# Performance work log

Hardware: AMD Instinct MI355X
Metric: run time of the kernel (lower is better)

Reference implementation:

```python
import jax, jax.numpy as jnp
import numpy as np


def setup_inputs() -> dict:
    key = jax.random.key(0)
    k1, k2 = jax.random.split(key)
    B, N, D = 16, 2048, 256
    candidate_vector = jax.random.normal(k1, (B, N, D), dtype=jnp.float32)
    # lengths in [1, N] so every softmax row has at least one valid column
    length = jax.random.randint(k2, (B,), 1, N + 1, dtype=jnp.int64)
    return {"candidate_vector": candidate_vector, "length": length}


def reference(candidate_vector, length):
    # scores[b,i,j] = <x_bi, x_bj>   (B, N, N)
    scores = jnp.einsum('bid,bjd->bij', candidate_vector, candidate_vector)
    # torch mask: mask[b,i,j] = (j < length[b]) -> columns past length masked
    N = candidate_vector.shape[1]
    col_valid = jnp.arange(N)[None, None, :] < length[:, None, None]  # (B,1,N)->(B,N,N) broadcast
    scores = jnp.where(col_valid, scores, -jnp.inf)
    weights = jax.nn.softmax(scores, axis=2)
    return jnp.einsum('bij,bjd->bid', weights, candidate_vector)
```

## Files before the change

kernel.cpp:

```cpp
#include <hip/hip_runtime.h>
#include <hip/hip_fp16.h>
#include <math.h>

typedef _Float16 f16;
typedef __attribute__((ext_vector_type(8))) _Float16 f16x8;
typedef __attribute__((ext_vector_type(4))) _Float16 f16x4;
typedef __attribute__((ext_vector_type(4))) float f32x4;

#define NB 16
#define NN 2048
#define ND 256
#define KVB 32
#define QB 64
#define XSZ ((size_t)NB * NN * ND)

__device__ __forceinline__ void gll16(const void* g, void* l) {
    __builtin_amdgcn_global_load_lds(
        (const __attribute__((address_space(1))) unsigned int*)g,
        (__attribute__((address_space(3))) unsigned int*)l, 16, 0, 0);
}

__device__ __forceinline__ long long len_at(const int* lenp, int b, bool is64) {
    return is64 ? ((const long long*)lenp)[b] : (long long)lenp[b];
}

__device__ __forceinline__ float bperm_f(int src_lane, float v) {
    return __int_as_float(__builtin_amdgcn_ds_bpermute(src_lane * 4, __float_as_int(v)));
}

__global__ __launch_bounds__(256)
void prep(const float* __restrict__ X, f16* __restrict__ Xh, f16* __restrict__ Xt)
{
    const int b  = blockIdx.z;
    const int n0 = blockIdx.x * 64;
    const int d0 = blockIdx.y * 64;
    const int t  = threadIdx.x;
    __shared__ f16 T[64][72];

    const float* Xb  = X  + ((size_t)b*NN + n0)*ND + d0;
    f16*         Xhb = Xh + ((size_t)b*NN + n0)*ND + d0;
    #pragma unroll
    for (int it = 0; it < 4; ++it) {
        int r  = it*16 + (t >> 4);
        int c4 = t & 15;
        float4 v = *(const float4*)(Xb + (size_t)r*ND + c4*4);
        f16x4 h; h[0]=(f16)v.x; h[1]=(f16)v.y; h[2]=(f16)v.z; h[3]=(f16)v.w;
        *(f16x4*)&Xhb[(size_t)r*ND + c4*4] = h;
        *(f16x4*)&T[r][c4*4] = h;
    }
    __syncthreads();
    f16* Xtb = Xt + ((size_t)b*ND + d0)*NN + n0;
    #pragma unroll
    for (int it = 0; it < 2; ++it) {
        int id = it*256 + t;
        int dr = id >> 3;
        int ch = id & 7;
        f16x8 v;
        #pragma unroll
        for (int u = 0; u < 8; ++u) v[u] = T[ch*8+u][dr];
        *(f16x8*)&Xtb[(size_t)dr*NN + ch*8] = v;
    }
}

__global__ __launch_bounds__(256, 2)
void attn8(const f16* __restrict__ Xh, const f16* __restrict__ Xt,
           const int* __restrict__ lenp,
           f16* __restrict__ Op, float* __restrict__ Sl)
{
    const int tid  = threadIdx.x;
    const int lane = tid & 63;
    const int w = tid >> 6;
    const int g = lane >> 4;
    const int c = lane & 15;

    const bool is64 = (lenp[1] == 0);
    long long Lv[NB];
    #pragma unroll
    for (int i = 0; i < NB; ++i) Lv[i] = len_at(lenp, i, is64);
    const int x   = blockIdx.x & 7;
    const int kk2 = blockIdx.x >> 3;
    const int h   = kk2 & 1;
    const int k2  = kk2 >> 1;
    const int wanted = (k2 < 32) ? x : (15 - x);
    const int qt  = k2 & 31;
    int bsel = 0; long long Lb = 1;
    #pragma unroll
    for (int bb = 0; bb < NB; ++bb) {
        int rk = 0;
        #pragma unroll
        for (int b2 = 0; b2 < NB; ++b2)
            rk += (Lv[b2] > Lv[bb]) || (Lv[b2] == Lv[bb] && b2 < bb);
        if (rk == wanted) { bsel = bb; Lb = Lv[bb]; }
    }
    const int nt  = (int)((Lb + KVB - 1) / KVB);
    const int nth = (h == 0) ? ((nt + 1) >> 1) : (nt >> 1);
    if (nth == 0) return;

    __shared__ f16 Kl[8192];
    __shared__ f16 Vl[8192];
    __shared__ f16 Pl[4][16*40];

    const char* xhb = (const char*)(Xh + (size_t)bsel*NN*ND);
    const char* xtb = (const char*)(Xt + (size_t)bsel*ND*NN);

    f16x8 qf[8];
    {
        const char* qp = xhb + (size_t)(qt*QB + w*16 + c)*512 + g*16;
        #pragma unroll
        for (int kk = 0; kk < 8; ++kk) qf[kk] = *(const f16x8*)(qp + kk*64);
    }

    auto stage_k = [&](int kv0) {
        char* kb = (char*)&Kl[0];
        #pragma unroll
        for (int it = 0; it < 4; ++it) {
            int S  = it*256 + tid;
            int kk = S >> 7, j = (S >> 2) & 31, gg = S & 3;
            gll16(xhb + (size_t)(kv0 + j)*512 + kk*64 + gg*16, kb + S*16);
        }
    };
    auto stage_v = [&](int kv0) {
        char* vb = (char*)&Vl[0];
        #pragma unroll
        for (int it = 0; it < 4; ++it) {
            int T  = it*256 + tid;
            int dt = T >> 6, cc = (T >> 2) & 15, gg = T & 3;
            gll16(xtb + (size_t)(dt*16 + cc)*4096 + (size_t)(kv0 + gg*8)*2, vb + T*16);
        }
    };

    f32x4 o[16];
    #pragma unroll
    for (int dt = 0; dt < 16; ++dt) o[dt] = (f32x4){0.f,0.f,0.f,0.f};
    float m = -INFINITY;
    float l = 0.f;

    f16* pw = &Pl[w][0];

    stage_k(h*KVB);
    stage_v(h*KVB);

    for (int ti = 0; ti < nth; ++ti) {
        const int kv0 = (2*ti + h) * KVB;
        const bool more = (ti + 1 < nth);

        asm volatile("s_waitcnt vmcnt(4)" ::: "memory");
        __builtin_amdgcn_s_barrier();

        const char* kb = (const char*)&Kl[0];
        const char* vb = (const char*)&Vl[0];

        f32x4 s0 = (f32x4){0.f,0.f,0.f,0.f};
        f32x4 s1 = (f32x4){0.f,0.f,0.f,0.f};
        __builtin_amdgcn_s_setprio(1);
        #pragma unroll
        for (int kk = 0; kk < 8; ++kk) {
            f16x8 b0 = *(const f16x8*)(kb + kk*2048        + c*64 + g*16);
            f16x8 b1 = *(const f16x8*)(kb + kk*2048 + 1024 + c*64 + g*16);
            s0 = __builtin_amdgcn_mfma_f32_16x16x32_f16(b0, qf[kk], s0, 0, 0, 0);
            s1 = __builtin_amdgcn_mfma_f32_16x16x32_f16(b1, qf[kk], s1, 0, 0, 0);
        }
        __builtin_amdgcn_s_setprio(0);

        asm volatile("s_waitcnt vmcnt(0)" ::: "memory");
        __builtin_amdgcn_s_barrier();
        if (more) stage_k(kv0 + 2*KVB);

        const float NEG = -1e30f;
        if (kv0 + KVB > (int)Lb) {
            const int jb = kv0 + g*4;
            #pragma unroll
            for (int r = 0; r < 4; ++r) {
                if (jb + r >= Lb)      s0[r] = NEG;
                if (jb + 16 + r >= Lb) s1[r] = NEG;
            }
        }

        float tm = fmaxf(fmaxf(fmaxf(s0[0],s0[1]), fmaxf(s0[2],s0[3])),
                         fmaxf(fmaxf(s1[0],s1[1]), fmaxf(s1[2],s1[3])));
        tm = fmaxf(tm, __shfl_xor(tm, 16, 64));
        tm = fmaxf(tm, __shfl_xor(tm, 32, 64));
        if (__any(tm > m + 8.f)) {
            float mn = fmaxf(m, tm);
            float sc = __expf(m - mn);
            m = mn; l *= sc;
            float scr[4];
            #pragma unroll
            for (int r = 0; r < 4; ++r) scr[r] = bperm_f(g*4 + r, sc);
            #pragma unroll
            for (int dt = 0; dt < 16; ++dt) {
                o[dt][0]*=scr[0]; o[dt][1]*=scr[1]; o[dt][2]*=scr[2]; o[dt][3]*=scr[3];
            }
        }
        float p0[4], p1[4];
        #pragma unroll
        for (int r = 0; r < 4; ++r) {
            p0[r] = __expf(s0[r] - m);
            p1[r] = __expf(s1[r] - m);
        }
        float rs = ((p0[0]+p0[1]) + (p0[2]+p0[3])) + ((p1[0]+p1[1]) + (p1[2]+p1[3]));
        rs += __shfl_xor(rs, 16, 64);
        rs += __shfl_xor(rs, 32, 64);
        l += rs;

        f16x4 pa, pb;
        pa[0]=(f16)p0[0]; pa[1]=(f16)p0[1]; pa[2]=(f16)p0[2]; pa[3]=(f16)p0[3];
        pb[0]=(f16)p1[0]; pb[1]=(f16)p1[1]; pb[2]=(f16)p1[2]; pb[3]=(f16)p1[3];
        *(f16x4*)&pw[c*40 + 4*g]      = pa;
        *(f16x4*)&pw[c*40 + 16 + 4*g] = pb;
        f16x8 pf = *(const f16x8*)&pw[c*40 + 8*g];

        __builtin_amdgcn_s_setprio(1);
        #pragma unroll
        for (int dt = 0; dt < 16; ++dt) {
            f16x8 vf = *(const f16x8*)(vb + dt*1024 + c*64 + g*16);
            o[dt] = __builtin_amdgcn_mfma_f32_16x16x32_f16(pf, vf, o[dt], 0, 0, 0);
        }
        __builtin_amdgcn_s_setprio(0);

        asm volatile("" ::: "memory");
        __builtin_amdgcn_s_barrier();
        if (more) stage_v(kv0 + 2*KVB);
    }

    float linv = 1.f / l;
    float inv[4];
    #pragma unroll
    for (int r = 0; r < 4; ++r) inv[r] = bperm_f(g*4 + r, linv);
    f16* op = Op + (size_t)h*XSZ + ((size_t)bsel*NN + (size_t)(qt*QB + w*16 + g*4))*ND + c;
    #pragma unroll
    for (int r = 0; r < 4; ++r) {
        #pragma unroll
        for (int dt = 0; dt < 16; ++dt)
            op[(size_t)r*ND + dt*16] = (f16)(o[dt][r] * inv[r]);
    }
    if (g == 0) {
        Sl[((size_t)(h*NB + bsel))*NN + (size_t)(qt*QB + w*16 + c)] = m + __logf(l);
    }
}

__global__ __launch_bounds__(256)
void merge(const f16* __restrict__ Op, const float* __restrict__ Sl,
           const int* __restrict__ lenp, float* __restrict__ out)
{
    const int tid = threadIdx.x;
    const int rg  = blockIdx.x * 8 + (tid >> 5);
    const int b   = rg >> 11;
    const int q   = rg & 2047;
    const int d0  = (tid & 31) * 8;

    const bool is64 = (lenp[1] == 0);
    const long long Lb = len_at(lenp, b, is64);

    const f16* p1 = Op + ((size_t)b*NN + q)*ND + d0;
    f16x8 a1 = *(const f16x8*)p1;
    float r[8];
    if (Lb <= KVB) {
        #pragma unroll
        for (int i = 0; i < 8; ++i) r[i] = (float)a1[i];
    } else {
        f16x8 a2 = *(const f16x8*)(p1 + XSZ);
        float s1 = Sl[(size_t)b*NN + q];
        float s2 = Sl[(size_t)(NB + b)*NN + q];
        float sm = fmaxf(s1, s2);
        float w1 = __expf(s1 - sm), w2 = __expf(s2 - sm);
        float dn = 1.f / (w1 + w2);
        w1 *= dn; w2 *= dn;
        #pragma unroll
        for (int i = 0; i < 8; ++i) r[i] = (float)a1[i]*w1 + (float)a2[i]*w2;
    }
    float* ob = out + ((size_t)b*NN + q)*ND + d0;
    *(float4*)ob       = (float4){r[0], r[1], r[2], r[3]};
    *(float4*)(ob + 4) = (float4){r[4], r[5], r[6], r[7]};
}

__global__ __launch_bounds__(256, 2)
void attn4(const f16* __restrict__ Xh, const f16* __restrict__ Xt,
           const int* __restrict__ lenp, float* __restrict__ out)
{
    const int tid  = threadIdx.x;
    const int lane = tid & 63;
    const int w = tid >> 6;
    const int g = lane >> 4;
    const int c = lane & 15;

    const bool is64 = (lenp[1] == 0);
    long long Lv[NB];
    #pragma unroll
    for (int i = 0; i < NB; ++i) Lv[i] = len_at(lenp, i, is64);
    const int x = blockIdx.x & 7;
    const int k = blockIdx.x >> 3;
    const int wanted = (k < 32) ? x : (15 - x);
    const int qt = k & 31;
    int bsel = 0; long long Lb = 1;
    #pragma unroll
    for (int bb = 0; bb < NB; ++bb) {
        int rk = 0;
        #pragma unroll
        for (int b2 = 0; b2 < NB; ++b2)
            rk += (Lv[b2] > Lv[bb]) || (Lv[b2] == Lv[bb] && b2 < bb);
        if (rk == wanted) { bsel = bb; Lb = Lv[bb]; }
    }
    const int nt = (int)((Lb + KVB - 1) / KVB);

    __shared__ f16 Kl[2][8192];
    __shared__ f16 Vl[2][8192];
    __shared__ f16 Pl[4][16*36];

    const char* xhb = (const char*)(Xh + (size_t)bsel*NN*ND);
    const char* xtb = (const char*)(Xt + (size_t)bsel*ND*NN);

    f16x8 qf[8];
    {
        const char* qp = xhb + (size_t)(qt*QB + w*16 + c)*512 + g*16;
        #pragma unroll
        for (int kk = 0; kk < 8; ++kk) qf[kk] = *(const f16x8*)(qp + kk*64);
    }

    auto stage = [&](int buf, int kv0) {
        char* kb = (char*)&Kl[buf][0];
        char* vb = (char*)&Vl[buf][0];
        #pragma unroll
        for (int it = 0; it < 4; ++it) {
            int S  = it*256 + tid;
            int kk = S >> 7, j = (S >> 2) & 31, gg = S & 3;
            gll16(xhb + (size_t)(kv0 + j)*512 + kk*64 + gg*16, kb + S*16);
        }
        #pragma unroll
        for (int it = 0; it < 4; ++it) {
            int T  = it*256 + tid;
            int dt = T >> 6, cc = (T >> 2) & 15, gg = T & 3;
            gll16(xtb + (size_t)(dt*16 + cc)*4096 + (size_t)(kv0 + gg*8)*2, vb + T*16);
        }
    };

    f32x4 o[16];
    #pragma unroll
    for (int dt = 0; dt < 16; ++dt) o[dt] = (f32x4){0.f,0.f,0.f,0.f};
    float m[4] = {-INFINITY,-INFINITY,-INFINITY,-INFINITY};
    float l[4] = {0.f,0.f,0.f,0.f};

    f16* pw = &Pl[w][0];

    stage(0, 0);
    if (nt > 1) stage(1, KVB);

    for (int t = 0; t < nt; ++t) {
        const int kv0 = t * KVB;
        const int buf = t & 1;

        if (t + 1 < nt) { asm volatile("s_waitcnt vmcnt(8)" ::: "memory"); }
        else            { asm volatile("s_waitcnt vmcnt(0)" ::: "memory"); }
        __builtin_amdgcn_s_barrier();

        const char* kb = (const char*)&Kl[buf][0];
        const char* vb = (const char*)&Vl[buf][0];

        f32x4 s0 = (f32x4){0.f,0.f,0.f,0.f};
        f32x4 s1 = (f32x4){0.f,0.f,0.f,0.f};
        #pragma unroll
        for (int kk = 0; kk < 8; ++kk) {
            f16x8 b0 = *(const f16x8*)(kb + kk*2048        + c*64 + g*16);
            f16x8 b1 = *(const f16x8*)(kb + kk*2048 + 1024 + c*64 + g*16);
            s0 = __builtin_amdgcn_mfma_f32_16x16x32_f16(qf[kk], b0, s0, 0, 0, 0);
            s1 = __builtin_amdgcn_mfma_f32_16x16x32_f16(qf[kk], b1, s1, 0, 0, 0);
        }

        const float NEG = -1e30f;
        if (kv0 + c >= Lb)      { s0[0]=NEG; s0[1]=NEG; s0[2]=NEG; s0[3]=NEG; }
        if (kv0 + 16 + c >= Lb) { s1[0]=NEG; s1[1]=NEG; s1[2]=NEG; s1[3]=NEG; }

        float mx[4], mn[4], sc[4], p0[4], p1[4], rs[4];
        #pragma unroll
        for (int r = 0; r < 4; ++r) mx[r] = fmaxf(s0[r], s1[r]);
        #pragma unroll
        for (int off = 8; off >= 1; off >>= 1) {
            #pragma unroll
            for (int r = 0; r < 4; ++r)
                mx[r] = fmaxf(mx[r], __shfl_xor(mx[r], off, 64));
        }
        #pragma unroll
        for (int r = 0; r < 4; ++r) {
            mn[r] = fmaxf(m[r], mx[r]);
            sc[r] = __expf(m[r] - mn[r]);
            p0[r] = __expf(s0[r] - mn[r]);
            p1[r] = __expf(s1[r] - mn[r]);
            rs[r] = p0[r] + p1[r];
        }
        #pragma unroll
        for (int off = 8; off >= 1; off >>= 1) {
            #pragma unroll
            for (int r = 0; r < 4; ++r)
                rs[r] += __shfl_xor(rs[r], off, 64);
        }
        bool chg = (sc[0]!=1.f) | (sc[1]!=1.f) | (sc[2]!=1.f) | (sc[3]!=1.f);
        if (__any(chg)) {
            #pragma unroll
            for (int dt = 0; dt < 16; ++dt) {
                o[dt][0]*=sc[0]; o[dt][1]*=sc[1]; o[dt][2]*=sc[2]; o[dt][3]*=sc[3];
            }
        }
        #pragma unroll
        for (int r = 0; r < 4; ++r) { l[r] = l[r]*sc[r] + rs[r]; m[r] = mn[r]; }

        #pragma unroll
        for (int r = 0; r < 4; ++r) {
            pw[(g*4+r)*36 + c]      = (f16)p0[r];
            pw[(g*4+r)*36 + 16 + c] = (f16)p1[r];
        }
        union { f16x4 hh[2]; f16x8 v; } pu;
        pu.hh[0] = *(const f16x4*)(pw + c*36 + g*8);
        pu.hh[1] = *(const f16x4*)(pw + c*36 + g*8 + 4);
        f16x8 pf = pu.v;

        #pragma unroll
        for (int dt = 0; dt < 16; ++dt) {
            f16x8 vf = *(const f16x8*)(vb + dt*1024 + c*64 + g*16);
            o[dt] = __builtin_amdgcn_mfma_f32_16x16x32_f16(pf, vf, o[dt], 0, 0, 0);
        }

        __builtin_amdgcn_s_barrier();
        if (t + 2 < nt) stage(buf, kv0 + 2*KVB);
    }

    float inv[4];
    #pragma unroll
    for (int r = 0; r < 4; ++r) inv[r] = 1.0f / l[r];
    float* ob = out + ((size_t)bsel*NN + (size_t)(qt*QB + w*16 + g*4))*ND + c;
    #pragma unroll
    for (int r = 0; r < 4; ++r) {
        #pragma unroll
        for (int dt = 0; dt < 16; ++dt)
            ob[(size_t)r*ND + dt*16] = o[dt][r] * inv[r];
    }
}

__global__ __launch_bounds__(256, 2)
void attn_fb(const float* __restrict__ X,
             const int* __restrict__ lenp,
             float* __restrict__ out)
{
    const int b   = blockIdx.y;
    const int qt  = blockIdx.x;
    const int tid = threadIdx.x;
    const int lane = tid & 63;
    const int w = tid >> 6;
    const int g = lane >> 4;
    const int c = lane & 15;

    const bool is64 = (lenp[1] == 0);
    const long long Lb = len_at(lenp, b, is64);

    __shared__ f16 Kl[KVB][264];
    __shared__ f16 Vt2[ND][40];
    __shared__ f16 Pl[4][16][40];

    const float* Xb = X + (size_t)b * NN * ND;

    f16x8 qf[8];
    {
        const float* qp = Xb + (size_t)(qt*64 + w*16 + c) * ND + g*8;
        #pragma unroll
        for (int kk = 0; kk < 8; ++kk) {
            float4 a = *(const float4*)(qp + kk*32);
            float4 d = *(const float4*)(qp + kk*32 + 4);
            f16x8 v;
            v[0]=(f16)a.x; v[1]=(f16)a.y; v[2]=(f16)a.z; v[3]=(f16)a.w;
            v[4]=(f16)d.x; v[5]=(f16)d.y; v[6]=(f16)d.z; v[7]=(f16)d.w;
            qf[kk] = v;
        }
    }

    f32x4 o[16];
    #pragma unroll
    for (int dt = 0; dt < 16; ++dt) o[dt] = (f32x4){0.f,0.f,0.f,0.f};
    float m[4] = {-INFINITY,-INFINITY,-INFINITY,-INFINITY};
    float lr[4] = {0.f,0.f,0.f,0.f};

    const int ntiles = (int)((Lb + KVB - 1) / KVB);
    for (int t = 0; t < ntiles; ++t) {
        const int kv0 = t * KVB;
        __syncthreads();
        #pragma unroll
        for (int it = 0; it < 8; ++it) {
            int idx4 = it*256 + tid;
            int row  = idx4 >> 6;
            int c4   = idx4 & 63;
            float4 v = *(const float4*)(Xb + (size_t)(kv0 + row)*ND + c4*4);
            f16x4 hh; hh[0]=(f16)v.x; hh[1]=(f16)v.y; hh[2]=(f16)v.z; hh[3]=(f16)v.w;
            *(f16x4*)&Kl[row][c4*4] = hh;
        }
        {
            const float* cp = Xb + (size_t)kv0*ND + tid;
            #pragma unroll
            for (int kq = 0; kq < 8; ++kq) {
                f16x4 hh;
                #pragma unroll
                for (int u = 0; u < 4; ++u) hh[u] = (f16)cp[(size_t)(kq*4+u)*ND];
                *(f16x4*)&Vt2[tid][kq*4] = hh;
            }
        }
        __syncthreads();

        f32x4 s0 = (f32x4){0.f,0.f,0.f,0.f};
        f32x4 s1 = (f32x4){0.f,0.f,0.f,0.f};
        #pragma unroll
        for (int kk = 0; kk < 8; ++kk) {
            f16x8 b0 = *(const f16x8*)&Kl[c     ][kk*32 + g*8];
            f16x8 b1 = *(const f16x8*)&Kl[16 + c][kk*32 + g*8];
            s0 = __builtin_amdgcn_mfma_f32_16x16x32_f16(qf[kk], b0, s0, 0, 0, 0);
            s1 = __builtin_amdgcn_mfma_f32_16x16x32_f16(qf[kk], b1, s1, 0, 0, 0);
        }

        const float NEG = -1e30f;
        if (kv0 + c >= Lb)      { s0[0]=NEG; s0[1]=NEG; s0[2]=NEG; s0[3]=NEG; }
        if (kv0 + 16 + c >= Lb) { s1[0]=NEG; s1[1]=NEG; s1[2]=NEG; s1[3]=NEG; }

        float mx[4], mn[4], sc[4], p0[4], p1[4], rs[4];
        #pragma unroll
        for (int r = 0; r < 4; ++r) mx[r] = fmaxf(s0[r], s1[r]);
        #pragma unroll
        for (int off = 8; off >= 1; off >>= 1) {
            #pragma unroll
            for (int r = 0; r < 4; ++r)
                mx[r] = fmaxf(mx[r], __shfl_xor(mx[r], off, 64));
        }
        #pragma unroll
        for (int r = 0; r < 4; ++r) {
            mn[r] = fmaxf(m[r], mx[r]);
            sc[r] = __expf(m[r] - mn[r]);
            p0[r] = __expf(s0[r] - mn[r]);
            p1[r] = __expf(s1[r] - mn[r]);
            rs[r] = p0[r] + p1[r];
        }
        #pragma unroll
        for (int off = 8; off >= 1; off >>= 1) {
            #pragma unroll
            for (int r = 0; r < 4; ++r)
                rs[r] += __shfl_xor(rs[r], off, 64);
        }
        bool chg = (sc[0]!=1.f) | (sc[1]!=1.f) | (sc[2]!=1.f) | (sc[3]!=1.f);
        if (__any(chg)) {
            #pragma unroll
            for (int dt = 0; dt < 16; ++dt) {
                o[dt][0]*=sc[0]; o[dt][1]*=sc[1]; o[dt][2]*=sc[2]; o[dt][3]*=sc[3];
            }
        }
        #pragma unroll
        for (int r = 0; r < 4; ++r) { lr[r] = lr[r]*sc[r] + rs[r]; m[r] = mn[r]; }

        #pragma unroll
        for (int r = 0; r < 4; ++r) {
            Pl[w][g*4+r][c]      = (f16)p0[r];
            Pl[w][g*4+r][16 + c] = (f16)p1[r];
        }
        f16x8 pf = *(const f16x8*)&Pl[w][c][g*8];

        #pragma unroll
        for (int dt = 0; dt < 16; ++dt) {
            f16x8 vf = *(const f16x8*)&Vt2[dt*16 + c][g*8];
            o[dt] = __builtin_amdgcn_mfma_f32_16x16x32_f16(pf, vf, o[dt], 0, 0, 0);
        }
    }

    float inv[4];
    #pragma unroll
    for (int r = 0; r < 4; ++r) inv[r] = 1.0f / lr[r];
    float* ob = out + ((size_t)b*NN + (size_t)(qt*64 + w*16 + g*4))*ND + c;
    #pragma unroll
    for (int r = 0; r < 4; ++r) {
        #pragma unroll
        for (int dt = 0; dt < 16; ++dt)
            ob[(size_t)r*ND + dt*16] = o[dt][r] * inv[r];
    }
}

extern "C" void kernel_launch(void* const* d_in, const int* in_sizes, int n_in,
                              void* d_out, int out_size, void* d_ws, size_t ws_size,
                              hipStream_t stream) {
    const float* X    = (const float*)d_in[0];
    const int*   lenp = (const int*)d_in[1];
    float*       out  = (float*)d_out;

    const size_t need_base  = XSZ * 2 * 2;
    const size_t need_split = need_base + XSZ * 2 * 2
                              + (size_t)2 * NB * NN * 4;
    if (ws_size >= need_split) {
        f16* Xh = (f16*)d_ws;
        f16* Xt = Xh + XSZ;
        f16* Op = Xt + XSZ;
        float* Sl = (float*)(Op + 2*XSZ);
        hipLaunchKernelGGL(prep, dim3(NN/64, ND/64, NB), dim3(256), 0, stream, X, Xh, Xt);
        hipLaunchKernelGGL(attn8, dim3(1024), dim3(256), 0, stream, Xh, Xt, lenp, Op, Sl);
        hipLaunchKernelGGL(merge, dim3(NB*NN/8), dim3(256), 0, stream, Op, Sl, lenp, out);
    } else if (ws_size >= need_base) {
        f16* Xh = (f16*)d_ws;
        f16* Xt = Xh + XSZ;
        hipLaunchKernelGGL(prep, dim3(NN/64, ND/64, NB), dim3(256), 0, stream, X, Xh, Xt);
        hipLaunchKernelGGL(attn4, dim3(512), dim3(256), 0, stream, Xh, Xt, lenp, out);
    } else {
        hipLaunchKernelGGL(attn_fb, dim3(NN/64, NB), dim3(256), 0, stream, X, lenp, out);
    }
}
```

Measured before the change: 96.57 us.

## Switch split-KV attention to 32x32x16 MFMA tiles with register P exchange

Replaces the 16x16x32 MFMA attention kernel with one built on 32x32x16 MFMAs. Each wave now owns 32 query rows, so a block covers 128 queries and the grid is halved to 512 blocks with launch bounds of one block per SM. The K/V LDS staging layouts are changed to match, and the probability matrix is exchanged between half-waves with cross-lane shuffles instead of going through LDS. The goal is fewer LDS reads per FLOP and no P round-trip through LDS, at the cost of higher register pressure (more Q fragments and accumulators) and less parallelism and occupancy.

```diff
diff --git a/kernel.cpp b/kernel.cpp
--- a/kernel.cpp
+++ b/kernel.cpp
@@ -6,12 +6,13 @@
 typedef __attribute__((ext_vector_type(8))) _Float16 f16x8;
 typedef __attribute__((ext_vector_type(4))) _Float16 f16x4;
 typedef __attribute__((ext_vector_type(4))) float f32x4;
+typedef __attribute__((ext_vector_type(16))) float f32x16;
+typedef unsigned int u32;
 
 #define NB 16
 #define NN 2048
 #define ND 256
 #define KVB 32
-#define QB 64
 #define XSZ ((size_t)NB * NN * ND)
 
 __device__ __forceinline__ void gll16(const void* g, void* l) {
@@ -62,16 +63,16 @@
     }
 }
 
-__global__ __launch_bounds__(256, 2)
-void attn8(const f16* __restrict__ Xh, const f16* __restrict__ Xt,
+__global__ __launch_bounds__(256, 1)
+void attn9(const f16* __restrict__ Xh, const f16* __restrict__ Xt,
            const int* __restrict__ lenp,
            f16* __restrict__ Op, float* __restrict__ Sl)
 {
     const int tid  = threadIdx.x;
     const int lane = tid & 63;
-    const int w = tid >> 6;
-    const int g = lane >> 4;
-    const int c = lane & 15;
+    const int w  = tid >> 6;
+    const int cl = lane & 31;
+    const int hi = lane >> 5;
 
     const bool is64 = (lenp[1] == 0);
     long long Lv[NB];
@@ -81,8 +82,8 @@
     const int kk2 = blockIdx.x >> 3;
     const int h   = kk2 & 1;
     const int k2  = kk2 >> 1;
-    const int wanted = (k2 < 32) ? x : (15 - x);
-    const int qt  = k2 & 31;
+    const int wanted = (k2 < 16) ? x : (15 - x);
+    const int qt  = k2 & 15;
     int bsel = 0; long long Lb = 1;
     #pragma unroll
     for (int bb = 0; bb < NB; ++bb) {
@@ -98,16 +99,17 @@
 
     __shared__ f16 Kl[8192];
     __shared__ f16 Vl[8192];
-    __shared__ f16 Pl[4][16*40];
 
     const char* xhb = (const char*)(Xh + (size_t)bsel*NN*ND);
     const char* xtb = (const char*)(Xt + (size_t)bsel*ND*NN);
 
-    f16x8 qf[8];
+    const int q0 = qt*128 + w*32;
+
+    f16x8 qf[16];
     {
-        const char* qp = xhb + (size_t)(qt*QB + w*16 + c)*512 + g*16;
-        #pragma unroll
-        for (int kk = 0; kk < 8; ++kk) qf[kk] = *(const f16x8*)(qp + kk*64);
+        const char* qp = xhb + (size_t)(q0 + cl)*512 + hi*16;
+        #pragma unroll
+        for (int kk = 0; kk < 16; ++kk) qf[kk] = *(const f16x8*)(qp + kk*32);
     }
 
     auto stage_k = [&](int kv0) {
@@ -115,8 +117,8 @@
         #pragma unroll
         for (int it = 0; it < 4; ++it) {
             int S  = it*256 + tid;
-            int kk = S >> 7, j = (S >> 2) & 31, gg = S & 3;
-            gll16(xhb + (size_t)(kv0 + j)*512 + kk*64 + gg*16, kb + S*16);
+            int kk = S >> 6, j = (S >> 1) & 31, h2 = S & 1;
+            gll16(xhb + (size_t)(kv0 + j)*512 + kk*32 + h2*16, kb + S*16);
         }
     };
     auto stage_v = [&](int kv0) {
@@ -124,18 +126,20 @@
         #pragma unroll
         for (int it = 0; it < 4; ++it) {
             int T  = it*256 + tid;
-            int dt = T >> 6, cc = (T >> 2) & 15, gg = T & 3;
-            gll16(xtb + (size_t)(dt*16 + cc)*4096 + (size_t)(kv0 + gg*8)*2, vb + T*16);
+            int ds = T >> 6, cc = (T >> 1) & 31, h2 = T & 1;
+            int dt = ds >> 1, s = ds & 1;
+            gll16(xtb + (size_t)(dt*32 + cc)*4096 + (size_t)(kv0 + s*16 + h2*8)*2,
+                  vb + T*16);
         }
     };
 
-    f32x4 o[16];
-    #pragma unroll
-    for (int dt = 0; dt < 16; ++dt) o[dt] = (f32x4){0.f,0.f,0.f,0.f};
+    f32x16 o[8];
+    #pragma unroll
+    for (int dt = 0; dt < 8; ++dt)
+        #pragma unroll
+        for (int r = 0; r < 16; ++r) o[dt][r] = 0.f;
     float m = -INFINITY;
     float l = 0.f;
-
-    f16* pw = &Pl[w][0];
 
     stage_k(h*KVB);
     stage_v(h*KVB);
@@ -150,15 +154,14 @@
         const char* kb = (const char*)&Kl[0];
         const char* vb = (const char*)&Vl[0];
 
-        f32x4 s0 = (f32x4){0.f,0.f,0.f,0.f};
-        f32x4 s1 = (f32x4){0.f,0.f,0.f,0.f};
+        f32x16 st;
+        #pragma unroll
+        for (int r = 0; r < 16; ++r) st[r] = 0.f;
         __builtin_amdgcn_s_setprio(1);
         #pragma unroll
-        for (int kk = 0; kk < 8; ++kk) {
-            f16x8 b0 = *(const f16x8*)(kb + kk*2048        + c*64 + g*16);
-            f16x8 b1 = *(const f16x8*)(kb + kk*2048 + 1024 + c*64 + g*16);
-            s0 = __builtin_amdgcn_mfma_f32_16x16x32_f16(b0, qf[kk], s0, 0, 0, 0);
-            s1 = __builtin_amdgcn_mfma_f32_16x16x32_f16(b1, qf[kk], s1, 0, 0, 0);
+        for (int kk = 0; kk < 16; ++kk) {
+            f16x8 ka = *(const f16x8*)(kb + kk*1024 + cl*32 + hi*16);
+            st = __builtin_amdgcn_mfma_f32_32x32x16_f16(ka, qf[kk], st, 0, 0, 0);
         }
         __builtin_amdgcn_s_setprio(0);
 
@@ -168,53 +171,67 @@
 
         const float NEG = -1e30f;
         if (kv0 + KVB > (int)Lb) {
-            const int jb = kv0 + g*4;
-            #pragma unroll
-            for (int r = 0; r < 4; ++r) {
-                if (jb + r >= Lb)      s0[r] = NEG;
-                if (jb + 16 + r >= Lb) s1[r] = NEG;
+            #pragma unroll
+            for (int r = 0; r < 16; ++r) {
+                int j = kv0 + (r & 3) + 8*(r >> 2) + 4*hi;
+                if (j >= (int)Lb) st[r] = NEG;
             }
         }
 
-        float tm = fmaxf(fmaxf(fmaxf(s0[0],s0[1]), fmaxf(s0[2],s0[3])),
-                         fmaxf(fmaxf(s1[0],s1[1]), fmaxf(s1[2],s1[3])));
-        tm = fmaxf(tm, __shfl_xor(tm, 16, 64));
+        float tm = st[0];
+        #pragma unroll
+        for (int r = 1; r < 16; ++r) tm = fmaxf(tm, st[r]);
         tm = fmaxf(tm, __shfl_xor(tm, 32, 64));
         if (__any(tm > m + 8.f)) {
             float mn = fmaxf(m, tm);
             float sc = __expf(m - mn);
             m = mn; l *= sc;
-            float scr[4];
-            #pragma unroll
-            for (int r = 0; r < 4; ++r) scr[r] = bperm_f(g*4 + r, sc);
-            #pragma unroll
-            for (int dt = 0; dt < 16; ++dt) {
-                o[dt][0]*=scr[0]; o[dt][1]*=scr[1]; o[dt][2]*=scr[2]; o[dt][3]*=scr[3];
-            }
-        }
-        float p0[4], p1[4];
-        #pragma unroll
-        for (int r = 0; r < 4; ++r) {
-            p0[r] = __expf(s0[r] - m);
-            p1[r] = __expf(s1[r] - m);
-        }
-        float rs = ((p0[0]+p0[1]) + (p0[2]+p0[3])) + ((p1[0]+p1[1]) + (p1[2]+p1[3]));
-        rs += __shfl_xor(rs, 16, 64);
+            float scr[16];
+            #pragma unroll
+            for (int r = 0; r < 16; ++r)
+                scr[r] = bperm_f((r & 3) + 8*(r >> 2) + 4*hi, sc);
+            #pragma unroll
+            for (int dt = 0; dt < 8; ++dt)
+                #pragma unroll
+                for (int r = 0; r < 16; ++r) o[dt][r] *= scr[r];
+        }
+        float p[16];
+        float rs = 0.f;
+        #pragma unroll
+        for (int r = 0; r < 16; ++r) { p[r] = __expf(st[r] - m); rs += p[r]; }
         rs += __shfl_xor(rs, 32, 64);
         l += rs;
 
-        f16x4 pa, pb;
-        pa[0]=(f16)p0[0]; pa[1]=(f16)p0[1]; pa[2]=(f16)p0[2]; pa[3]=(f16)p0[3];
-        pb[0]=(f16)p1[0]; pb[1]=(f16)p1[1]; pb[2]=(f16)p1[2]; pb[3]=(f16)p1[3];
-        *(f16x4*)&pw[c*40 + 4*g]      = pa;
-        *(f16x4*)&pw[c*40 + 16 + 4*g] = pb;
-        f16x8 pf = *(const f16x8*)&pw[c*40 + 8*g];
+        u32 pk[8];
+        #pragma unroll
+        for (int Q = 0; Q < 4; ++Q) {
+            f16x4 t;
+            t[0]=(f16)p[4*Q+0]; t[1]=(f16)p[4*Q+1];
+            t[2]=(f16)p[4*Q+2]; t[3]=(f16)p[4*Q+3];
+            pk[2*Q]   = ((u32*)&t)[0];
+            pk[2*Q+1] = ((u32*)&t)[1];
+        }
+        u32 rx0 = __shfl_xor(hi ? pk[0] : pk[2], 32, 64);
+        u32 rx1 = __shfl_xor(hi ? pk[1] : pk[3], 32, 64);
+        u32 rx2 = __shfl_xor(hi ? pk[4] : pk[6], 32, 64);
+        u32 rx3 = __shfl_xor(hi ? pk[5] : pk[7], 32, 64);
+        union { u32 u[4]; f16x8 v; } pf0, pf1;
+        pf0.u[0] = hi ? rx0 : pk[0];
+        pf0.u[1] = hi ? rx1 : pk[1];
+        pf0.u[2] = hi ? pk[2] : rx0;
+        pf0.u[3] = hi ? pk[3] : rx1;
+        pf1.u[0] = hi ? rx2 : pk[4];
+        pf1.u[1] = hi ? rx3 : pk[5];
+        pf1.u[2] = hi ? pk[6] : rx2;
+        pf1.u[3] = hi ? pk[7] : rx3;
 
         __builtin_amdgcn_s_setprio(1);
         #pragma unroll
-        for (int dt = 0; dt < 16; ++dt) {
-            f16x8 vf = *(const f16x8*)(vb + dt*1024 + c*64 + g*16);
-            o[dt] = __builtin_amdgcn_mfma_f32_16x16x32_f16(pf, vf, o[dt], 0, 0, 0);
+        for (int dt = 0; dt < 8; ++dt) {
+            f16x8 v0 = *(const f16x8*)(vb + (dt*2    )*1024 + cl*32 + hi*16);
+            f16x8 v1 = *(const f16x8*)(vb + (dt*2 + 1)*1024 + cl*32 + hi*16);
+            o[dt] = __builtin_amdgcn_mfma_f32_32x32x16_f16(pf0.v, v0, o[dt], 0, 0, 0);
+            o[dt] = __builtin_amdgcn_mfma_f32_32x32x16_f16(pf1.v, v1, o[dt], 0, 0, 0);
         }
         __builtin_amdgcn_s_setprio(0);
 
@@ -224,18 +241,18 @@
     }
 
     float linv = 1.f / l;
-    float inv[4];
-    #pragma unroll
-    for (int r = 0; r < 4; ++r) inv[r] = bperm_f(g*4 + r, linv);
-    f16* op = Op + (size_t)h*XSZ + ((size_t)bsel*NN + (size_t)(qt*QB + w*16 + g*4))*ND + c;
-    #pragma unroll
-    for (int r = 0; r < 4; ++r) {
-        #pragma unroll
-        for (int dt = 0; dt < 16; ++dt)
-            op[(size_t)r*ND + dt*16] = (f16)(o[dt][r] * inv[r]);
-    }
-    if (g == 0) {
-        Sl[((size_t)(h*NB + bsel))*NN + (size_t)(qt*QB + w*16 + c)] = m + __logf(l);
+    f16* opb = Op + (size_t)h*XSZ + ((size_t)bsel*NN + q0)*ND;
+    #pragma unroll
+    for (int r = 0; r < 16; ++r) {
+        const int qr = (r & 3) + 8*(r >> 2) + 4*hi;
+        const float inv = bperm_f(qr, linv);
+        f16* row = opb + (size_t)qr*ND + cl;
+        #pragma unroll
+        for (int dt = 0; dt < 8; ++dt)
+            row[dt*32] = (f16)(o[dt][r] * inv);
+    }
+    if (hi == 0) {
+        Sl[((size_t)(h*NB + bsel))*NN + (size_t)(q0 + cl)] = m + __logf(l);
     }
 }
 
@@ -312,7 +329,7 @@
 
     f16x8 qf[8];
     {
-        const char* qp = xhb + (size_t)(qt*QB + w*16 + c)*512 + g*16;
+        const char* qp = xhb + (size_t)(qt*64 + w*16 + c)*512 + g*16;
         #pragma unroll
         for (int kk = 0; kk < 8; ++kk) qf[kk] = *(const f16x8*)(qp + kk*64);
     }
@@ -426,7 +443,7 @@
     float inv[4];
     #pragma unroll
     for (int r = 0; r < 4; ++r) inv[r] = 1.0f / l[r];
-    float* ob = out + ((size_t)bsel*NN + (size_t)(qt*QB + w*16 + g*4))*ND + c;
+    float* ob = out + ((size_t)bsel*NN + (size_t)(qt*64 + w*16 + g*4))*ND + c;
     #pragma unroll
     for (int r = 0; r < 4; ++r) {
         #pragma unroll
@@ -591,7 +608,7 @@
         f16* Op = Xt + XSZ;
         float* Sl = (float*)(Op + 2*XSZ);
         hipLaunchKernelGGL(prep, dim3(NN/64, ND/64, NB), dim3(256), 0, stream, X, Xh, Xt);
-        hipLaunchKernelGGL(attn8, dim3(1024), dim3(256), 0, stream, Xh, Xt, lenp, Op, Sl);
+        hipLaunchKernelGGL(attn9, dim3(512), dim3(256), 0, stream, Xh, Xt, lenp, Op, Sl);
         hipLaunchKernelGGL(merge, dim3(NB*NN/8), dim3(256), 0, stream, Op, Sl, lenp, out);
     } else if (ws_size >= need_base) {
         f16* Xh = (f16*)d_ws;
```

Measured after the change: 125.4 us. +29.9%, slower.

## Swap P via ds_bpermute, raise occupancy, and reorder block schedule

Applied to the files above, without the earlier changes.

The softmax probability fragment is now moved between lanes with ds_bpermute instead of a round trip through shared memory, which removes the per-wave P scratch buffer. The launch bound is raised from 2 to 4 blocks per CU, trading register headroom for occupancy. Block-to-work assignment also changes to a serpentine ordering by length rank, so long and short batches are spread across launch waves. The risks are register spills under the tighter bound and eight bpermute ops replacing a single LDS store and load.

```diff
diff --git a/kernel.cpp b/kernel.cpp
--- a/kernel.cpp
+++ b/kernel.cpp
@@ -6,6 +6,7 @@
 typedef __attribute__((ext_vector_type(8))) _Float16 f16x8;
 typedef __attribute__((ext_vector_type(4))) _Float16 f16x4;
 typedef __attribute__((ext_vector_type(4))) float f32x4;
+typedef unsigned int u32;
 
 #define NB 16
 #define NN 2048
@@ -62,10 +63,10 @@
     }
 }
 
-__global__ __launch_bounds__(256, 2)
-void attn8(const f16* __restrict__ Xh, const f16* __restrict__ Xt,
-           const int* __restrict__ lenp,
-           f16* __restrict__ Op, float* __restrict__ Sl)
+__global__ __launch_bounds__(256, 4)
+void attn10(const f16* __restrict__ Xh, const f16* __restrict__ Xt,
+            const int* __restrict__ lenp,
+            f16* __restrict__ Op, float* __restrict__ Sl)
 {
     const int tid  = threadIdx.x;
     const int lane = tid & 63;
@@ -77,12 +78,13 @@
     long long Lv[NB];
     #pragma unroll
     for (int i = 0; i < NB; ++i) Lv[i] = len_at(lenp, i, is64);
-    const int x   = blockIdx.x & 7;
-    const int kk2 = blockIdx.x >> 3;
-    const int h   = kk2 & 1;
-    const int k2  = kk2 >> 1;
-    const int wanted = (k2 < 32) ? x : (15 - x);
-    const int qt  = k2 & 31;
+    const int i  = blockIdx.x;
+    const int rr = i >> 8;
+    const int ss = i & 255;
+    const int rank = rr*256 + ((rr & 1) ? (255 - ss) : ss);
+    const int brk = rank >> 6;
+    const int qt  = (rank >> 1) & 31;
+    const int h   = rank & 1;
     int bsel = 0; long long Lb = 1;
     #pragma unroll
     for (int bb = 0; bb < NB; ++bb) {
@@ -90,7 +92,7 @@
         #pragma unroll
         for (int b2 = 0; b2 < NB; ++b2)
             rk += (Lv[b2] > Lv[bb]) || (Lv[b2] == Lv[bb] && b2 < bb);
-        if (rk == wanted) { bsel = bb; Lb = Lv[bb]; }
+        if (rk == brk) { bsel = bb; Lb = Lv[bb]; }
     }
     const int nt  = (int)((Lb + KVB - 1) / KVB);
     const int nth = (h == 0) ? ((nt + 1) >> 1) : (nt >> 1);
@@ -98,7 +100,6 @@
 
     __shared__ f16 Kl[8192];
     __shared__ f16 Vl[8192];
-    __shared__ f16 Pl[4][16*40];
 
     const char* xhb = (const char*)(Xh + (size_t)bsel*NN*ND);
     const char* xtb = (const char*)(Xt + (size_t)bsel*ND*NN);
@@ -134,8 +135,6 @@
     for (int dt = 0; dt < 16; ++dt) o[dt] = (f32x4){0.f,0.f,0.f,0.f};
     float m = -INFINITY;
     float l = 0.f;
-
-    f16* pw = &Pl[w][0];
 
     stage_k(h*KVB);
     stage_v(h*KVB);
@@ -206,15 +205,31 @@
         f16x4 pa, pb;
         pa[0]=(f16)p0[0]; pa[1]=(f16)p0[1]; pa[2]=(f16)p0[2]; pa[3]=(f16)p0[3];
         pb[0]=(f16)p1[0]; pb[1]=(f16)p1[1]; pb[2]=(f16)p1[2]; pb[3]=(f16)p1[3];
-        *(f16x4*)&pw[c*40 + 4*g]      = pa;
-        *(f16x4*)&pw[c*40 + 16 + 4*g] = pb;
-        f16x8 pf = *(const f16x8*)&pw[c*40 + 8*g];
+        u32 a0 = ((u32*)&pa)[0], a1 = ((u32*)&pa)[1];
+        u32 b0_ = ((u32*)&pb)[0], b1_ = ((u32*)&pb)[1];
+        const bool lo = (g < 2);
+        const int gA   = lo ? (2*g) : (2*g - 4);
+        const int adrA = (gA*16 + c) * 4;
+        const int adrB = adrA + 64;
+        u32 xA0 = __builtin_amdgcn_ds_bpermute(adrA, a0);
+        u32 xA1 = __builtin_amdgcn_ds_bpermute(adrA, a1);
+        u32 yA0 = __builtin_amdgcn_ds_bpermute(adrA, b0_);
+        u32 yA1 = __builtin_amdgcn_ds_bpermute(adrA, b1_);
+        u32 xB0 = __builtin_amdgcn_ds_bpermute(adrB, a0);
+        u32 xB1 = __builtin_amdgcn_ds_bpermute(adrB, a1);
+        u32 yB0 = __builtin_amdgcn_ds_bpermute(adrB, b0_);
+        u32 yB1 = __builtin_amdgcn_ds_bpermute(adrB, b1_);
+        union { u32 u[4]; f16x8 v; } pf;
+        pf.u[0] = lo ? xA0 : yA0;
+        pf.u[1] = lo ? xA1 : yA1;
+        pf.u[2] = lo ? xB0 : yB0;
+        pf.u[3] = lo ? xB1 : yB1;
 
         __builtin_amdgcn_s_setprio(1);
         #pragma unroll
         for (int dt = 0; dt < 16; ++dt) {
             f16x8 vf = *(const f16x8*)(vb + dt*1024 + c*64 + g*16);
-            o[dt] = __builtin_amdgcn_mfma_f32_16x16x32_f16(pf, vf, o[dt], 0, 0, 0);
+            o[dt] = __builtin_amdgcn_mfma_f32_16x16x32_f16(pf.v, vf, o[dt], 0, 0, 0);
         }
         __builtin_amdgcn_s_setprio(0);
 
@@ -591,7 +606,7 @@
         f16* Op = Xt + XSZ;
         float* Sl = (float*)(Op + 2*XSZ);
         hipLaunchKernelGGL(prep, dim3(NN/64, ND/64, NB), dim3(256), 0, stream, X, Xh, Xt);
-        hipLaunchKernelGGL(attn8, dim3(1024), dim3(256), 0, stream, Xh, Xt, lenp, Op, Sl);
+        hipLaunchKernelGGL(attn10, dim3(1024), dim3(256), 0, stream, Xh, Xt, lenp, Op, Sl);
         hipLaunchKernelGGL(merge, dim3(NB*NN/8), dim3(256), 0, stream, Op, Sl, lenp, out);
     } else if (ws_size >= need_base) {
         f16* Xh = (f16*)d_ws;
```

Measured after the change: 175.6 us. 1.82x slower.
